# Performance work log

Measured on AMD Instinct MI355X. Metric: run time of the kernel, lower is better.

The kernel has to match this reference:

```python
import jax, jax.numpy as jnp
import numpy as np

NLAT = 192  # octahedral O96-class grid


def _lons(nlat):
    half = [20 + 4 * i for i in range(nlat // 2)]
    return half + half[::-1]


def _dft_matrix(nlat, mmax):
    # Truncated per-ring real-DFT basis (torch.fft.rfft convention, 'forward' 1/n norm).
    # Ring j has nlon_j points; frequencies beyond its Nyquist (m > nlon_j//2) are zero.
    lons = _lons(nlat)
    max_nlon = max(lons)
    D = np.zeros((nlat, max_nlon, mmax), dtype=np.complex64)
    for j, n in enumerate(lons):
        keep = min(mmax, n // 2 + 1)
        k = np.arange(n)[:, None]
        m = np.arange(keep)[None, :]
        D[j, :n, :keep] = np.exp(-2j * np.pi * k * m / n) / n
    return D


def _legendre_weights(nlat, lmax, mmax):
    # Orthonormalized associated Legendre P_l^m at Gaussian latitudes (north->south),
    # with Gaussian quadrature weights and the 2*pi longitude factor folded in.
    xg, wg = np.polynomial.legendre.leggauss(nlat)
    x = xg[::-1].copy()
    w = wg[::-1].copy()
    s = np.sqrt(1.0 - x * x)
    leg = np.zeros((lmax, mmax, nlat))
    pmm = np.full(nlat, 1.0 / np.sqrt(4.0 * np.pi))
    for m in range(mmax):
        if m > 0:
            pmm = -np.sqrt((2 * m + 1) / (2.0 * m)) * s * pmm
        if m < lmax:
            leg[m, m] = pmm
        if m + 1 < lmax:
            leg[m + 1, m] = np.sqrt(2 * m + 3.0) * x * pmm
        for l in range(m + 2, lmax):
            a = np.sqrt((4.0 * l * l - 1.0) / (l * l - m * m))
            bb = np.sqrt(((2.0 * l + 1.0) * (l - 1 + m) * (l - 1 - m)) / ((2.0 * l - 3.0) * (l * l - m * m)))
            leg[l, m] = a * x * leg[l - 1, m] - bb * leg[l - 2, m]
    leg = 2.0 * np.pi * leg * w[None, None, :]
    return leg.astype(np.float32)


def setup_inputs() -> dict:
    key = jax.random.key(0)
    nlat = NLAT
    lmax = mmax = nlat // 2
    n_points = sum(_lons(nlat))  # 40320 for nlat=192
    data = jax.random.normal(key, (4, 1, 1, n_points, 100), dtype=jnp.float32)
    dft = jnp.asarray(_dft_matrix(nlat, mmax))
    leg = jnp.asarray(_legendre_weights(nlat, lmax, mmax))
    return {"data": data, "dft": dft, "leg": leg}


def reference(data, dft, leg):
    b, t, e, p, v = data.shape
    nlat, max_nlon, mmax = dft.shape
    lmax = leg.shape[0]
    lons = _lons(nlat)
    # static scatter map: flattened ragged rings -> [nlat, max_nlon] padded layout
    flat_idx = np.concatenate([j * max_nlon + np.arange(n) for j, n in enumerate(lons)])
    x = jnp.transpose(data, (0, 1, 2, 4, 3)).reshape(-1, p)  # [(b t e v), p]
    B = x.shape[0]
    x_pad = jnp.zeros((B, nlat * max_nlon), x.dtype).at[:, flat_idx].set(x)
    x_pad = x_pad.reshape(B, nlat, max_nlon)
    # ragged per-ring truncated real DFT, then associated-Legendre contraction
    f_hat = jnp.einsum('bjn,jnm->bjm', x_pad, dft)        # [B, nlat, mmax] complex
    coeffs = jnp.einsum('bjm,lmj->blm', f_hat, leg)       # [B, lmax, mmax] complex
    coeffs = coeffs.reshape(b, t, e, v, lmax, mmax)
    return jnp.transpose(coeffs, (0, 1, 2, 4, 5, 3))      # [b, t, e, yF, xF, v]
```

## Files before the change

kernel.cpp:

```cpp
#include <hip/hip_runtime.h>

#define NLAT 192
#define NPTS 40320
#define MMAX 96
#define LMAX 96
#define NV   100
#define MAXN 400
#define NB   400

typedef __attribute__((ext_vector_type(8))) short short8v;
typedef __attribute__((ext_vector_type(4))) float f32x4;

#define ASTR 56
#define XSTR 56
#define FSTR 40

static __device__ __forceinline__ float bits2f(unsigned int b) {
    union { unsigned int i; float f; } v; v.i = b; return v.f;
}
static __device__ __forceinline__ unsigned int f2bf(float f) {
    union { float f; unsigned int i; } v; v.f = f;
    return (v.i + 0x7FFFu + ((v.i >> 16) & 1u)) >> 16;
}

__global__ __launch_bounds__(256) void leg_conv_kernel(
    const float* __restrict__ leg,
    unsigned short* __restrict__ legh,
    unsigned short* __restrict__ legl)
{
    int idx = blockIdx.x * 256 + threadIdx.x;
    if (idx >= 96 * 96 * 192) return;
    int j = idx % 192;
    int lm = idx / 192;
    int m = lm % 96, l = lm / 96;
    float v = leg[idx];
    unsigned int h = f2bf(v);
    unsigned int lo = f2bf(v - bits2f(h << 16));
    size_t o = ((size_t)m * 96 + l) * 192 + j;
    legh[o] = (unsigned short)h;
    legl[o] = (unsigned short)lo;
}

__global__ __launch_bounds__(256, 4) void dft_mfma_kernel(
    const float* __restrict__ data,
    const unsigned int* __restrict__ dftw,
    unsigned short* __restrict__ fh_hi,
    unsigned short* __restrict__ fh_lo,
    int c0, int cn)
{
    __shared__ short A_lds[192 * ASTR];
    __shared__ short Xh_lds[64 * XSTR];
    __shared__ short Xl_lds[64 * XSTR];

    const int bt  = blockIdx.x;
    const int p   = blockIdx.y;
    const int tid = threadIdx.x;
    const int w   = tid >> 6;
    const int l   = tid & 63;
    const int lr  = l & 15;
    const int kg  = l >> 4;

    const int Bb = c0 + bt * 50;
    const int bb = Bb / NV;
    const int vb = Bb % NV;
    const float* dbase = data + (size_t)bb * NPTS * NV + vb;

    for (int rr = 0; rr < 2; ++rr) {
        int j, n, start;
        if (rr == 0) { j = p;      n = 20 + 4 * p;  start = 2 * p * p + 18 * p; }
        else         { j = 96 + p; n = 400 - 4 * p; start = 20160 + 402 * p - 2 * p * p; }

        f32x4 acc[3][4];
#pragma unroll
        for (int i = 0; i < 3; ++i)
#pragma unroll
            for (int nt = 0; nt < 4; ++nt) acc[i][nt] = (f32x4){0.f, 0.f, 0.f, 0.f};

        for (int k0 = 0; k0 < n; k0 += 32) {
            __syncthreads();

#pragma unroll
            for (int s = 0; s < 3; ++s) {
                int q  = tid + 256 * s;
                int kq = q / 96;
                int m  = q - kq * 96;
                int kb = k0 + kq * 4;
                unsigned int w0 = 0, w1 = 0, w2 = 0, w3 = 0;
                const unsigned int* dp = dftw + ((size_t)j * MAXN + kb) * 96 + m;
                if (kb     < n) w0 = dp[0];
                if (kb + 1 < n) w1 = dp[96];
                if (kb + 2 < n) w2 = dp[192];
                if (kb + 3 < n) w3 = dp[288];
                uint2 re = { (w0 & 0xFFFFu) | (w1 << 16), (w2 & 0xFFFFu) | (w3 << 16) };
                uint2 im = { (w0 >> 16) | (w1 & 0xFFFF0000u), (w2 >> 16) | (w3 & 0xFFFF0000u) };
                *(uint2*)&A_lds[m * ASTR + kq * 4]        = re;
                *(uint2*)&A_lds[(96 + m) * ASTR + kq * 4] = im;
            }

#pragma unroll
            for (int s = 0; s < 4; ++s) {
                int q  = tid + 256 * s;
                int c  = q & 63;
                int kp = q >> 6;
                int k  = k0 + 2 * kp;
                float x0 = 0.f, x1 = 0.f;
                if (c < 50) {
                    const float* sp = dbase + (size_t)(start + k) * NV + c;
                    if (k     < n) x0 = sp[0];
                    if (k + 1 < n) x1 = sp[NV];
                }
                unsigned int h0 = f2bf(x0), h1 = f2bf(x1);
                float r0 = x0 - bits2f(h0 << 16);
                float r1 = x1 - bits2f(h1 << 16);
                unsigned int l0 = f2bf(r0), l1 = f2bf(r1);
                ((unsigned int*)Xh_lds)[c * (XSTR / 2) + kp] = h0 | (h1 << 16);
                ((unsigned int*)Xl_lds)[c * (XSTR / 2) + kp] = l0 | (l1 << 16);
            }
            __syncthreads();

            short8v a0 = *(const short8v*)&A_lds[((3 * w + 0) * 16 + lr) * ASTR + kg * 8];
            short8v a1 = *(const short8v*)&A_lds[((3 * w + 1) * 16 + lr) * ASTR + kg * 8];
            short8v a2 = *(const short8v*)&A_lds[((3 * w + 2) * 16 + lr) * ASTR + kg * 8];
#pragma unroll
            for (int nt = 0; nt < 4; ++nt) {
                short8v bh = *(const short8v*)&Xh_lds[(nt * 16 + lr) * XSTR + kg * 8];
                short8v bl = *(const short8v*)&Xl_lds[(nt * 16 + lr) * XSTR + kg * 8];
                acc[0][nt] = __builtin_amdgcn_mfma_f32_16x16x32_bf16(a0, bh, acc[0][nt], 0, 0, 0);
                acc[1][nt] = __builtin_amdgcn_mfma_f32_16x16x32_bf16(a1, bh, acc[1][nt], 0, 0, 0);
                acc[2][nt] = __builtin_amdgcn_mfma_f32_16x16x32_bf16(a2, bh, acc[2][nt], 0, 0, 0);
                acc[0][nt] = __builtin_amdgcn_mfma_f32_16x16x32_bf16(a0, bl, acc[0][nt], 0, 0, 0);
                acc[1][nt] = __builtin_amdgcn_mfma_f32_16x16x32_bf16(a1, bl, acc[1][nt], 0, 0, 0);
                acc[2][nt] = __builtin_amdgcn_mfma_f32_16x16x32_bf16(a2, bl, acc[2][nt], 0, 0, 0);
            }
        }

#pragma unroll
        for (int i = 0; i < 3; ++i)
#pragma unroll
            for (int nt = 0; nt < 4; ++nt) {
                int c = nt * 16 + lr;
                if (c < 50) {
                    int Brel = bt * 50 + c;
                    int mm0 = (3 * w + i) * 16 + kg * 4;
                    unsigned short* oh = fh_hi + ((size_t)j * 192 + mm0) * cn + Brel;
                    unsigned short* ol = fh_lo + ((size_t)j * 192 + mm0) * cn + Brel;
#pragma unroll
                    for (int r = 0; r < 4; ++r) {
                        float v = acc[i][nt][r];
                        unsigned int h = f2bf(v);
                        unsigned int lo = f2bf(v - bits2f(h << 16));
                        oh[(size_t)r * cn] = (unsigned short)h;
                        ol[(size_t)r * cn] = (unsigned short)lo;
                    }
                }
            }
    }
}

__global__ __launch_bounds__(256) void leg_mfma_kernel(
    const unsigned short* __restrict__ legh,
    const unsigned short* __restrict__ legl,
    const unsigned short* __restrict__ fh_hi,
    const unsigned short* __restrict__ fh_lo,
    unsigned int* __restrict__ out,
    int c0, int cn)
{
    __shared__ unsigned short A_lds[2 * 96 * FSTR];
    __shared__ unsigned short F_lds[2 * 2 * 64 * FSTR];

    const int m   = blockIdx.x;
    const int bt  = blockIdx.y;
    const int tid = threadIdx.x;
    const int w   = tid >> 6;
    const int l   = tid & 63;
    const int lr  = l & 15;
    const int kg  = l >> 4;

    f32x4 acc[6][2];
#pragma unroll
    for (int lt = 0; lt < 6; ++lt)
#pragma unroll
        for (int pl = 0; pl < 2; ++pl) acc[lt][pl] = (f32x4){0.f, 0.f, 0.f, 0.f};

    const unsigned int* lh32 = (const unsigned int*)legh;
    const unsigned int* ll32 = (const unsigned int*)legl;

    for (int j0 = 0; j0 < NLAT; j0 += 32) {
        __syncthreads();

#pragma unroll
        for (int s = 0; s < 12; ++s) {
            const int hl = (s >= 6) ? 1 : 0;
            int rem = tid + 256 * s - 1536 * hl;
            int lrow = rem >> 4;
            int ku = rem & 15;
            const unsigned int* src = hl ? ll32 : lh32;
            unsigned int v = src[((size_t)m * 96 + lrow) * 96 + (j0 >> 1) + ku];
            ((unsigned int*)A_lds)[(size_t)hl * 96 * (FSTR / 2) + lrow * (FSTR / 2) + ku] = v;
        }

#pragma unroll
        for (int s = 0; s < 13; ++s) {
            int q = tid + 256 * s;
            if (q < 3200) {
                int u  = q % 25;
                int r2 = q / 25;
                int jj = r2 & 31;
                int r3 = r2 >> 5;
                int pl = r3 & 1;
                int hl = r3 >> 1;
                const unsigned short* src = hl ? fh_lo : fh_hi;
                const unsigned int* s32 = (const unsigned int*)src;
                unsigned int v = s32[((size_t)(j0 + jj) * 192 + m + 96 * pl) * (cn >> 1)
                                     + bt * 25 + u];
                size_t base = ((size_t)(pl * 2 + hl) * 64 + 2 * u) * FSTR + jj;
                F_lds[base]        = (unsigned short)(v & 0xFFFFu);
                F_lds[base + FSTR] = (unsigned short)(v >> 16);
            }
        }
        __syncthreads();

        short8v fH[2], fL[2];
#pragma unroll
        for (int pl = 0; pl < 2; ++pl) {
            fH[pl] = *(const short8v*)&F_lds[((size_t)(pl * 2 + 0) * 64 + w * 16 + lr) * FSTR + kg * 8];
            fL[pl] = *(const short8v*)&F_lds[((size_t)(pl * 2 + 1) * 64 + w * 16 + lr) * FSTR + kg * 8];
        }
#pragma unroll
        for (int lt = 0; lt < 6; ++lt) {
            short8v ah = *(const short8v*)&A_lds[(size_t)(0 * 96 + lt * 16 + lr) * FSTR + kg * 8];
            short8v al = *(const short8v*)&A_lds[(size_t)(1 * 96 + lt * 16 + lr) * FSTR + kg * 8];
#pragma unroll
            for (int pl = 0; pl < 2; ++pl) {
                acc[lt][pl] = __builtin_amdgcn_mfma_f32_16x16x32_bf16(ah, fH[pl], acc[lt][pl], 0, 0, 0);
                acc[lt][pl] = __builtin_amdgcn_mfma_f32_16x16x32_bf16(ah, fL[pl], acc[lt][pl], 0, 0, 0);
                acc[lt][pl] = __builtin_amdgcn_mfma_f32_16x16x32_bf16(al, fH[pl], acc[lt][pl], 0, 0, 0);
            }
        }
    }

    int c = w * 16 + lr;
    if (c < 50) {
        int B = c0 + bt * 50 + c;
        int bb = B / NV, vv = B % NV;
#pragma unroll
        for (int lt = 0; lt < 6; ++lt) {
#pragma unroll
            for (int r = 0; r < 4; ++r) {
                int ll = lt * 16 + kg * 4 + r;
                out[(((size_t)bb * LMAX + ll) * MMAX + m) * NV + vv] =
                    f2bf(acc[lt][0][r]) | (f2bf(acc[lt][1][r]) << 16);
            }
        }
    }
}

extern "C" void kernel_launch(void* const* d_in, const int* in_sizes, int n_in,
                              void* d_out, int out_size, void* d_ws, size_t ws_size,
                              hipStream_t stream) {
    if (n_in != 3) return;

    const float* data = (const float*)d_in[0];
    const unsigned int* dftw = (const unsigned int*)d_in[1];
    const float* leg  = (const float*)d_in[2];
    unsigned int* out = (unsigned int*)d_out;

    const size_t LEGN = (size_t)96 * 96 * 192;
    const size_t LEGB = 2 * LEGN * sizeof(unsigned short);
    const size_t rowb = (size_t)192 * 192 * 2 * sizeof(unsigned short);
    if (ws_size < LEGB + 50 * rowb) return;

    unsigned short* legh = (unsigned short*)d_ws;
    unsigned short* legl = legh + LEGN;

    size_t maxrows = (ws_size - LEGB) / rowb;
    int chunk = (int)((maxrows / 50) * 50);
    if (chunk > NB) chunk = NB;

    leg_conv_kernel<<<dim3((96 * 96 * 192 + 255) / 256), dim3(256), 0, stream>>>(
        leg, legh, legl);

    for (int c0 = 0; c0 < NB; c0 += chunk) {
        int cn = NB - c0 < chunk ? NB - c0 : chunk;
        unsigned short* fh_hi = legl + LEGN;
        unsigned short* fh_lo = fh_hi + (size_t)192 * 192 * cn;

        dim3 g1(cn / 50, 96);
        dft_mfma_kernel<<<g1, dim3(256), 0, stream>>>(data, dftw, fh_hi, fh_lo, c0, cn);
        dim3 g2(96, cn / 50);
        leg_mfma_kernel<<<g2, dim3(256), 0, stream>>>(legh, legl, fh_hi, fh_lo, out, c0, cn);
    }
}
```

Measured before the change: 96.56 us.

## Pre-transpose DFT basis and stream it into LDS with direct global-to-LDS loads

Adds a prepass kernel that splits the packed complex bf16 DFT weights into a per-ring, k-padded, row-major re/im layout in workspace. The DFT MFMA kernel then fills its A tile with 16-byte global_load_lds transfers into an XOR-swizzled unpadded LDS layout instead of gathering and repacking through registers. The X staging is restructured so each thread loads 8 consecutive k values and builds the hi/lo bf16 split with a byte perm and v_cvt_pk_bf16_f32. The cost is an extra transpose kernel launch, more workspace, and a hi part that now truncates rather than rounds.

```diff
diff --git a/kernel.cpp b/kernel.cpp
--- a/kernel.cpp
+++ b/kernel.cpp
@@ -11,8 +11,6 @@
 typedef __attribute__((ext_vector_type(8))) short short8v;
 typedef __attribute__((ext_vector_type(4))) float f32x4;
 
-#define ASTR 56
-#define XSTR 56
 #define FSTR 40
 
 static __device__ __forceinline__ float bits2f(unsigned int b) {
@@ -21,6 +19,23 @@
 static __device__ __forceinline__ unsigned int f2bf(float f) {
     union { float f; unsigned int i; } v; v.f = f;
     return (v.i + 0x7FFFu + ((v.i >> 16) & 1u)) >> 16;
+}
+
+static __device__ __forceinline__ int Ssum(int n) {
+    int q = n >> 3, r = n & 7; return 4 * q * (q - 1) + q * r;
+}
+static __device__ __forceinline__ int atoffk(int j) {
+    if (j < 96) return 32 * (Ssum(j + 12) - 4);
+    return 32 * (672 + 676 - Ssum(204 - j));
+}
+static __device__ __forceinline__ int kpad_of(int j) {
+    return 32 * ((j < 96 ? (j + 12) : (203 - j)) >> 3);
+}
+
+typedef const __attribute__((address_space(1))) void* gas_ptr;
+typedef __attribute__((address_space(3))) void* las_ptr;
+static __device__ __forceinline__ void gload_lds16(const void* g, void* l) {
+    __builtin_amdgcn_global_load_lds((gas_ptr)g, (las_ptr)l, 16, 0, 0);
 }
 
 __global__ __launch_bounds__(256) void leg_conv_kernel(
@@ -41,16 +56,51 @@
     legl[o] = (unsigned short)lo;
 }
 
+__global__ __launch_bounds__(256) void dft_transpose_kernel(
+    const unsigned int* __restrict__ dftw,
+    unsigned short* __restrict__ At)
+{
+    const int j = blockIdx.x;
+    const int kpad = kpad_of(j);
+    const int k0 = blockIdx.y * 32;
+    if (k0 >= kpad) return;
+    const int n = j < 96 ? 20 + 4 * j : 400 - 4 * (j - 96);
+    unsigned short* abase = At + (size_t)atoffk(j) * 192;
+    const int tid = threadIdx.x;
+#pragma unroll
+    for (int s = 0; s < 3; ++s) {
+        int slot = s * 256 + tid;
+        int row = slot % 192;
+        int ch  = slot / 192;
+        int m = row < 96 ? row : row - 96;
+        bool isIm = row >= 96;
+        const unsigned int* dp = dftw + ((size_t)j * MAXN + k0 + ch * 8) * 96 + m;
+        unsigned short o[8];
+#pragma unroll
+        for (int i = 0; i < 8; ++i) {
+            int k = k0 + ch * 8 + i;
+            unsigned int v = (k < n) ? dp[(size_t)i * 96] : 0u;
+            o[i] = isIm ? (unsigned short)(v >> 16) : (unsigned short)(v & 0xFFFFu);
+        }
+        uint4 pk;
+        pk.x = (unsigned int)o[0] | ((unsigned int)o[1] << 16);
+        pk.y = (unsigned int)o[2] | ((unsigned int)o[3] << 16);
+        pk.z = (unsigned int)o[4] | ((unsigned int)o[5] << 16);
+        pk.w = (unsigned int)o[6] | ((unsigned int)o[7] << 16);
+        *(uint4*)(abase + (size_t)row * kpad + k0 + ch * 8) = pk;
+    }
+}
+
 __global__ __launch_bounds__(256, 4) void dft_mfma_kernel(
     const float* __restrict__ data,
-    const unsigned int* __restrict__ dftw,
+    const unsigned short* __restrict__ At,
     unsigned short* __restrict__ fh_hi,
     unsigned short* __restrict__ fh_lo,
     int c0, int cn)
 {
-    __shared__ short A_lds[192 * ASTR];
-    __shared__ short Xh_lds[64 * XSTR];
-    __shared__ short Xl_lds[64 * XSTR];
+    __shared__ unsigned short A_lds[192 * 32];
+    __shared__ unsigned short Xh_lds[64 * 32];
+    __shared__ unsigned short Xl_lds[64 * 32];
 
     const int bt  = blockIdx.x;
     const int p   = blockIdx.y;
@@ -59,16 +109,23 @@
     const int l   = tid & 63;
     const int lr  = l & 15;
     const int kg  = l >> 4;
+    const int kgp = kg ^ ((lr >> 1) & 3);
 
     const int Bb = c0 + bt * 50;
     const int bb = Bb / NV;
     const int vb = Bb % NV;
     const float* dbase = data + (size_t)bb * NPTS * NV + vb;
 
+    const int xc  = tid >> 2;
+    const int xch = tid & 3;
+    const int xpc = xch ^ ((xc >> 1) & 3);
+
     for (int rr = 0; rr < 2; ++rr) {
         int j, n, start;
         if (rr == 0) { j = p;      n = 20 + 4 * p;  start = 2 * p * p + 18 * p; }
         else         { j = 96 + p; n = 400 - 4 * p; start = 20160 + 402 * p - 2 * p * p; }
+        const int kpad = kpad_of(j);
+        const unsigned short* abase = At + (size_t)atoffk(j) * 192;
 
         f32x4 acc[3][4];
 #pragma unroll
@@ -76,55 +133,50 @@
 #pragma unroll
             for (int nt = 0; nt < 4; ++nt) acc[i][nt] = (f32x4){0.f, 0.f, 0.f, 0.f};
 
-        for (int k0 = 0; k0 < n; k0 += 32) {
+        for (int k0 = 0; k0 < kpad; k0 += 32) {
             __syncthreads();
 
 #pragma unroll
             for (int s = 0; s < 3; ++s) {
-                int q  = tid + 256 * s;
-                int kq = q / 96;
-                int m  = q - kq * 96;
-                int kb = k0 + kq * 4;
-                unsigned int w0 = 0, w1 = 0, w2 = 0, w3 = 0;
-                const unsigned int* dp = dftw + ((size_t)j * MAXN + kb) * 96 + m;
-                if (kb     < n) w0 = dp[0];
-                if (kb + 1 < n) w1 = dp[96];
-                if (kb + 2 < n) w2 = dp[192];
-                if (kb + 3 < n) w3 = dp[288];
-                uint2 re = { (w0 & 0xFFFFu) | (w1 << 16), (w2 & 0xFFFFu) | (w3 << 16) };
-                uint2 im = { (w0 >> 16) | (w1 & 0xFFFF0000u), (w2 >> 16) | (w3 & 0xFFFF0000u) };
-                *(uint2*)&A_lds[m * ASTR + kq * 4]        = re;
-                *(uint2*)&A_lds[(96 + m) * ASTR + kq * 4] = im;
-            }
-
-#pragma unroll
-            for (int s = 0; s < 4; ++s) {
-                int q  = tid + 256 * s;
-                int c  = q & 63;
-                int kp = q >> 6;
-                int k  = k0 + 2 * kp;
-                float x0 = 0.f, x1 = 0.f;
-                if (c < 50) {
-                    const float* sp = dbase + (size_t)(start + k) * NV + c;
-                    if (k     < n) x0 = sp[0];
-                    if (k + 1 < n) x1 = sp[NV];
+                int slot = s * 256 + tid;
+                int row  = slot >> 2;
+                int chL  = (slot & 3) ^ ((row >> 1) & 3);
+                const unsigned short* g = abase + (size_t)row * kpad + k0 + chL * 8;
+                gload_lds16(g, &A_lds[s * 2048 + w * 512]);
+            }
+
+            float xv[8];
+            {
+                const float* sp = dbase + (size_t)(start + k0 + xch * 8) * NV + xc;
+#pragma unroll
+                for (int i = 0; i < 8; ++i) {
+                    int k = k0 + xch * 8 + i;
+                    xv[i] = (xc < 50 && k < n) ? sp[(size_t)i * NV] : 0.f;
                 }
-                unsigned int h0 = f2bf(x0), h1 = f2bf(x1);
-                float r0 = x0 - bits2f(h0 << 16);
-                float r1 = x1 - bits2f(h1 << 16);
-                unsigned int l0 = f2bf(r0), l1 = f2bf(r1);
-                ((unsigned int*)Xh_lds)[c * (XSTR / 2) + kp] = h0 | (h1 << 16);
-                ((unsigned int*)Xl_lds)[c * (XSTR / 2) + kp] = l0 | (l1 << 16);
-            }
+            }
+            unsigned int hi4[4], lo4[4];
+#pragma unroll
+            for (int t2 = 0; t2 < 4; ++t2) {
+                unsigned int x0 = __float_as_uint(xv[2 * t2]);
+                unsigned int x1 = __float_as_uint(xv[2 * t2 + 1]);
+                hi4[t2] = __builtin_amdgcn_perm(x1, x0, 0x07060302u);
+                float r0 = xv[2 * t2]     - bits2f(x0 & 0xFFFF0000u);
+                float r1 = xv[2 * t2 + 1] - bits2f(x1 & 0xFFFF0000u);
+                unsigned int pk;
+                asm("v_cvt_pk_bf16_f32 %0, %1, %2" : "=v"(pk) : "v"(r0), "v"(r1));
+                lo4[t2] = pk;
+            }
+            *(uint4*)&Xh_lds[xc * 32 + xpc * 8] = (uint4){hi4[0], hi4[1], hi4[2], hi4[3]};
+            *(uint4*)&Xl_lds[xc * 32 + xpc * 8] = (uint4){lo4[0], lo4[1], lo4[2], lo4[3]};
             __syncthreads();
 
-            short8v a0 = *(const short8v*)&A_lds[((3 * w + 0) * 16 + lr) * ASTR + kg * 8];
-            short8v a1 = *(const short8v*)&A_lds[((3 * w + 1) * 16 + lr) * ASTR + kg * 8];
-            short8v a2 = *(const short8v*)&A_lds[((3 * w + 2) * 16 + lr) * ASTR + kg * 8];
+            short8v a0 = *(const short8v*)&A_lds[((3 * w + 0) * 16 + lr) * 32 + kgp * 8];
+            short8v a1 = *(const short8v*)&A_lds[((3 * w + 1) * 16 + lr) * 32 + kgp * 8];
+            short8v a2 = *(const short8v*)&A_lds[((3 * w + 2) * 16 + lr) * 32 + kgp * 8];
 #pragma unroll
             for (int nt = 0; nt < 4; ++nt) {
-                short8v bh = *(const short8v*)&Xh_lds[(nt * 16 + lr) * XSTR + kg * 8];
-                short8v bl = *(const short8v*)&Xl_lds[(nt * 16 + lr) * XSTR + kg * 8];
+                short8v bh = *(const short8v*)&Xh_lds[(nt * 16 + lr) * 32 + kgp * 8];
+                short8v bl = *(const short8v*)&Xl_lds[(nt * 16 + lr) * 32 + kgp * 8];
                 acc[0][nt] = __builtin_amdgcn_mfma_f32_16x16x32_bf16(a0, bh, acc[0][nt], 0, 0, 0);
                 acc[1][nt] = __builtin_amdgcn_mfma_f32_16x16x32_bf16(a1, bh, acc[1][nt], 0, 0, 0);
                 acc[2][nt] = __builtin_amdgcn_mfma_f32_16x16x32_bf16(a2, bh, acc[2][nt], 0, 0, 0);
@@ -267,26 +319,30 @@
 
     const size_t LEGN = (size_t)96 * 96 * 192;
     const size_t LEGB = 2 * LEGN * sizeof(unsigned short);
+    const size_t ATN  = (size_t)43008 * 192;
+    const size_t ATB  = ATN * sizeof(unsigned short);
     const size_t rowb = (size_t)192 * 192 * 2 * sizeof(unsigned short);
-    if (ws_size < LEGB + 50 * rowb) return;
+    if (ws_size < LEGB + ATB + 50 * rowb) return;
 
     unsigned short* legh = (unsigned short*)d_ws;
     unsigned short* legl = legh + LEGN;
-
-    size_t maxrows = (ws_size - LEGB) / rowb;
+    unsigned short* At   = legl + LEGN;
+
+    size_t maxrows = (ws_size - LEGB - ATB) / rowb;
     int chunk = (int)((maxrows / 50) * 50);
     if (chunk > NB) chunk = NB;
 
     leg_conv_kernel<<<dim3((96 * 96 * 192 + 255) / 256), dim3(256), 0, stream>>>(
         leg, legh, legl);
+    dft_transpose_kernel<<<dim3(192, 13), dim3(256), 0, stream>>>(dftw, At);
 
     for (int c0 = 0; c0 < NB; c0 += chunk) {
         int cn = NB - c0 < chunk ? NB - c0 : chunk;
-        unsigned short* fh_hi = legl + LEGN;
+        unsigned short* fh_hi = At + ATN;
         unsigned short* fh_lo = fh_hi + (size_t)192 * 192 * cn;
 
         dim3 g1(cn / 50, 96);
-        dft_mfma_kernel<<<g1, dim3(256), 0, stream>>>(data, dftw, fh_hi, fh_lo, c0, cn);
+        dft_mfma_kernel<<<g1, dim3(256), 0, stream>>>(data, At, fh_hi, fh_lo, c0, cn);
         dim3 g2(96, cn / 50);
         leg_mfma_kernel<<<g2, dim3(256), 0, stream>>>(legh, legl, fh_hi, fh_lo, out, c0, cn);
     }
```

Result: slower. 105.3 us (+9.0%).
